# Kernel tuning notes

Hardware: AMD Instinct MI355X
Metric: run time of the kernel (lower is better)

## Reference

```python
import jax, jax.numpy as jnp
import numpy as np

NUM_HEADS = 16
LN_EPS = 1e-05


def setup_inputs() -> dict:
    key = jax.random.key(0)
    ks = jax.random.split(key, 10)
    B, S, H = 2, 2048, 1024
    s = 1.0 / np.sqrt(H)
    return {
        "hidden_states": jax.random.normal(ks[0], (B, S, H), dtype=jnp.float32),
        "Wq": jax.random.normal(ks[1], (H, H), dtype=jnp.float32) * s,
        "bq": jax.random.normal(ks[2], (H,), dtype=jnp.float32) * 0.02,
        "Wk": jax.random.normal(ks[3], (H, H), dtype=jnp.float32) * s,
        "bk": jax.random.normal(ks[4], (H,), dtype=jnp.float32) * 0.02,
        "Wv": jax.random.normal(ks[5], (H, H), dtype=jnp.float32) * s,
        "bv": jax.random.normal(ks[6], (H,), dtype=jnp.float32) * 0.02,
        "Wd": jax.random.normal(ks[7], (H, H), dtype=jnp.float32) * s,
        "bd": jax.random.normal(ks[8], (H,), dtype=jnp.float32) * 0.02,
        "ln_gamma": jnp.ones((H,), dtype=jnp.float32),
        "ln_beta": jnp.zeros((H,), dtype=jnp.float32),
    }


def reference(hidden_states, Wq, bq, Wk, bk, Wv, bv, Wd, bd, ln_gamma, ln_beta):
    B, S, H = hidden_states.shape
    nh = NUM_HEADS
    hd = H // nh

    # QKV projections (torch Linear: x @ W.T + b), split heads -> [B, nh, S, hd]
    def proj(W, b):
        y = jnp.einsum('bsh,oh->bso', hidden_states, W) + b
        return y.reshape(B, S, nh, hd).transpose(0, 2, 1, 3)

    q = proj(Wq, bq)
    k = proj(Wk, bk)
    v = proj(Wv, bv)

    # scaled dot-product attention: [B, nh, S, S]
    scores = jnp.einsum('bhqd,bhkd->bhqk', q, k) / jnp.sqrt(jnp.float32(hd))
    probs = jax.nn.softmax(scores, axis=-1)
    ctx = jnp.einsum('bhqk,bhkd->bhqd', probs, v)  # [B, nh, S, hd]
    ctx = ctx.transpose(0, 2, 1, 3).reshape(B, S, H)

    # output dense + residual + LayerNorm
    attn_out = jnp.einsum('bsh,oh->bso', ctx, Wd) + bd
    x = attn_out + hidden_states
    mu = jnp.mean(x, axis=-1, keepdims=True)
    var = jnp.mean(jnp.square(x - mu), axis=-1, keepdims=True)
    return (x - mu) * jax.lax.rsqrt(var + LN_EPS) * ln_gamma + ln_beta
```

## Files before the change

### kernel.cpp

```cpp
#include <hip/hip_runtime.h>

constexpr int kH    = 1024;
constexpr int kSEQ  = 2048;
constexpr int kBATCH= 2;
constexpr int kNH   = 16;
constexpr int kHD   = 64;
constexpr int kM    = 4096;

typedef _Float16 h8  __attribute__((ext_vector_type(8)));
typedef _Float16 h4  __attribute__((ext_vector_type(4)));
typedef float   f32x4 __attribute__((ext_vector_type(4)));

static __device__ __forceinline__ f32x4 mfma16(h8 a, h8 b, f32x4 c) {
  return __builtin_amdgcn_mfma_f32_16x16x32_f16(a, b, c, 0, 0, 0);
}

static __device__ __forceinline__ void gll16(const _Float16* g, _Float16* l) {
  __builtin_amdgcn_global_load_lds(
      (const __attribute__((address_space(1))) void*)g,
      (__attribute__((address_space(3))) void*)l, 16, 0, 0);
}

#define QSCALE 0.18033688011112042f
#define C0INIT (-5.770780163555854f)

__global__ __launch_bounds__(256) void cvt_all(
    const float* __restrict__ X,  const float* __restrict__ Wq,
    const float* __restrict__ Wk, const float* __restrict__ Wv,
    const float* __restrict__ Wd,
    _Float16* __restrict__ Xh,  _Float16* __restrict__ Wqh,
    _Float16* __restrict__ Wkh, _Float16* __restrict__ Wvh,
    _Float16* __restrict__ Wdh)
{
  int i = blockIdx.x * 256 + threadIdx.x;
  const float* src; _Float16* dst; int off;
  if (i < (kM * kH) / 4) {
    src = X; dst = Xh; off = i;
  } else {
    int j = i - (kM * kH) / 4;
    int w = j >> 18;
    off = j & 262143;
    src = (w == 0) ? Wq : (w == 1) ? Wk : (w == 2) ? Wv : Wd;
    dst = (w == 0) ? Wqh : (w == 1) ? Wkh : (w == 2) ? Wvh : Wdh;
  }
  float4 v = reinterpret_cast<const float4*>(src)[off];
  h4 o;
  o[0] = (_Float16)v.x; o[1] = (_Float16)v.y;
  o[2] = (_Float16)v.z; o[3] = (_Float16)v.w;
  reinterpret_cast<h4*>(dst)[off] = o;
}

__global__ __launch_bounds__(256, 2) void qkv_gemm(
    const _Float16* __restrict__ Xh,
    const _Float16* __restrict__ Wq, const _Float16* __restrict__ Wk,
    const _Float16* __restrict__ Wv,
    const float* __restrict__ bq, const float* __restrict__ bk,
    const float* __restrict__ bv,
    _Float16* __restrict__ Qo, _Float16* __restrict__ Ko, _Float16* __restrict__ Vo)
{
  const int proj = blockIdx.z;
  const _Float16* W   = (proj == 0) ? Wq : ((proj == 1) ? Wk : Wv);
  const float*    bias= (proj == 0) ? bq : ((proj == 1) ? bk : bv);
  _Float16*       Out = (proj == 0) ? Qo : ((proj == 1) ? Ko : Vo);

  const int m0 = blockIdx.y * 128, n0 = blockIdx.x * 128;
  __shared__ __align__(16) char qsmem[32768];
  _Float16* const As = (_Float16*)qsmem;
  _Float16* const Bs = (_Float16*)(qsmem + 16384);
  _Float16* const Lt = (_Float16*)qsmem;

  const int tid  = threadIdx.x;
  const int wave = tid >> 6, lane = tid & 63, quad = lane >> 4, l16 = lane & 15;
  const int mw = (wave & 1) * 64, nw = (wave >> 1) * 64;

  f32x4 acc[4][4] = {};
  const int grow = wave * 32 + (lane >> 2);
  const int gcol = (lane & 3) * 8;
  const _Float16* Ag = Xh + (size_t)(m0 + grow) * kH + gcol;
  const _Float16* Bg = W  + (size_t)(n0 + grow) * kH + gcol;

  {
    gll16(Ag,            &As[wave * 1024]);
    gll16(Ag + 16 * kH,  &As[wave * 1024 + 512]);
    gll16(Bg,            &Bs[wave * 1024]);
    gll16(Bg + 16 * kH,  &Bs[wave * 1024 + 512]);
  }

  for (int k = 0; k < 32; ++k) {
    const int cur = k & 1;
    __syncthreads();
    if (k < 31) {
      const int k0 = (k + 1) * 32, nb = cur ^ 1;
      gll16(Ag + k0,           &As[nb * 4096 + wave * 1024]);
      gll16(Ag + 16 * kH + k0, &As[nb * 4096 + wave * 1024 + 512]);
      gll16(Bg + k0,           &Bs[nb * 4096 + wave * 1024]);
      gll16(Bg + 16 * kH + k0, &Bs[nb * 4096 + wave * 1024 + 512]);
    }
    h8 af[4], bf[4];
    #pragma unroll
    for (int mi = 0; mi < 4; ++mi)
      af[mi] = *reinterpret_cast<const h8*>(&As[cur * 4096 + (mw + mi * 16 + l16) * 32 + quad * 8]);
    #pragma unroll
    for (int ni = 0; ni < 4; ++ni)
      bf[ni] = *reinterpret_cast<const h8*>(&Bs[cur * 4096 + (nw + ni * 16 + l16) * 32 + quad * 8]);
    #pragma unroll
    for (int mi = 0; mi < 4; ++mi)
      #pragma unroll
      for (int ni = 0; ni < 4; ++ni)
        acc[mi][ni] = mfma16(af[mi], bf[ni], acc[mi][ni]);
  }

  if (proj != 2) {
    #pragma unroll
    for (int mi = 0; mi < 4; ++mi)
    #pragma unroll
    for (int ni = 0; ni < 4; ++ni) {
      const int ng = n0 + nw + ni * 16 + l16;
      const float bv_ = bias[ng];
      const int hh = ng >> 6, dd = ng & 63;
      #pragma unroll
      for (int r = 0; r < 4; ++r) {
        const int mg = m0 + mw + mi * 16 + quad * 4 + r;
        float val = acc[mi][ni][r] + bv_;
        if (proj == 0) val *= QSCALE;
        const int bb = mg >> 11, srow = mg & 2047;
        Out[(((size_t)(bb * kNH + hh) * kSEQ) + srow) * kHD + dd] = (_Float16)val;
      }
    }
  } else {
    __syncthreads();
    #pragma unroll
    for (int mi = 0; mi < 4; ++mi)
    #pragma unroll
    for (int ni = 0; ni < 4; ++ni) {
      const int ng = n0 + nw + ni * 16 + l16;
      const float bv_ = bias[ng];
      const int nl = nw + ni * 16 + l16;
      const int c16 = (mw >> 3) + mi * 2 + (quad >> 1);
      const int cs = c16 ^ (nl & 15);
      h4 pp;
      pp[0] = (_Float16)(acc[mi][ni][0] + bv_);
      pp[1] = (_Float16)(acc[mi][ni][1] + bv_);
      pp[2] = (_Float16)(acc[mi][ni][2] + bv_);
      pp[3] = (_Float16)(acc[mi][ni][3] + bv_);
      *reinterpret_cast<h4*>(&Lt[nl * 128 + cs * 8 + (quad & 1) * 4]) = pp;
    }
    __syncthreads();
    const int bb = m0 >> 11, srow0 = m0 & 2047;
    const int nl2 = tid >> 1, half = tid & 1;
    const int ng2 = n0 + nl2, hh2 = ng2 >> 6, dd2 = ng2 & 63;
    _Float16* dst = Out + ((size_t)(bb * kNH + hh2) * kHD + dd2) * kSEQ
                        + srow0 + half * 64;
    #pragma unroll
    for (int j = 0; j < 8; ++j) {
      const int c = half * 8 + j;
      const int cs = c ^ (nl2 & 15);
      *reinterpret_cast<h8*>(dst + j * 8) =
          *reinterpret_cast<const h8*>(&Lt[nl2 * 128 + cs * 8]);
    }
  }
}

__global__ __launch_bounds__(512, 4) void attn_kernel(
    const _Float16* __restrict__ Q, const _Float16* __restrict__ K,
    const _Float16* __restrict__ Vt, _Float16* __restrict__ Ctx)
{
  const int qt = blockIdx.x, bh = blockIdx.y;
  const int tid = threadIdx.x;
  const int wave = tid >> 6, lane = tid & 63, quad = lane >> 4, l16 = lane & 15;
  const int sw = l16 & 7;
  const int qw = wave & 3;
  const int wg = wave >> 2;

  __shared__ __align__(16) char smem[61440];
  _Float16* const Kl = (_Float16*)smem;
  _Float16* const Vl = (_Float16*)(smem + 16384);
  _Float16* const Pl = (_Float16*)(smem + 32768);
  float* const Ored = (float*)smem;
  float* const Lred = (float*)(smem + 34816);

  const _Float16* Qb = Q  + (size_t)bh * kSEQ * kHD;
  const _Float16* Kb = K  + (size_t)bh * kSEQ * kHD;
  const _Float16* Vb = Vt + (size_t)bh * kHD * kSEQ;

  const int qbase = qt * 128 + qw * 32;
  h8 qf[2][2];
  #pragma unroll
  for (int qh = 0; qh < 2; ++qh)
    #pragma unroll
    for (int dh = 0; dh < 2; ++dh)
      qf[qh][dh] = *reinterpret_cast<const h8*>(
          &Qb[(size_t)(qbase + qh * 16 + l16) * kHD + dh * 32 + quad * 8]);

  const int srow0  = lane >> 3;
  const int schunk = (lane & 7) ^ srow0;
  const int krow   = wave * 8 + srow0;
  const _Float16* Kg = Kb + (size_t)krow * kHD + schunk * 8;
  const _Float16* Vg = Vb + (size_t)krow * kSEQ + schunk * 8;
  _Float16* const PlW = Pl + wave * 1792;

  float l_acc[2] = {0.f, 0.f};
  f32x4 o[2][4] = {};

  gll16(Kg, &Kl[(wave * 8) * 64]);
  gll16(Vg, &Vl[(wave * 8) * 64]);

  for (int kt = 0; kt < kSEQ / 64; ++kt) {
    const int cur = kt & 1;
    __syncthreads();
    if (kt + 1 < kSEQ / 64) {
      const int nb = cur ^ 1;
      const size_t ko = (size_t)(kt + 1) * 64;
      gll16(Kg + ko * kHD, &Kl[nb * 4096 + (wave * 8) * 64]);
      gll16(Vg + ko,       &Vl[nb * 4096 + (wave * 8) * 64]);
    }
    const _Float16* Kc = Kl + cur * 4096;
    const _Float16* Vc = Vl + cur * 4096;

    h8 ka[2][2];
    #pragma unroll
    for (int nt = 0; nt < 2; ++nt) {
      const int keyl = wg * 32 + nt * 16 + l16;
      ka[nt][0] = *reinterpret_cast<const h8*>(&Kc[keyl * 64 + ((quad    ) ^ sw) * 8]);
      ka[nt][1] = *reinterpret_cast<const h8*>(&Kc[keyl * 64 + ((quad ^ 4) ^ sw) * 8]);
    }
    f32x4 s[2][2];
    __builtin_amdgcn_s_setprio(1);
    #pragma unroll
    for (int nt = 0; nt < 2; ++nt)
      #pragma unroll
      for (int qh = 0; qh < 2; ++qh) {
        f32x4 a = {C0INIT, C0INIT, C0INIT, C0INIT};
        a = mfma16(ka[nt][0], qf[qh][0], a);
        a = mfma16(ka[nt][1], qf[qh][1], a);
        s[nt][qh] = a;
      }
    __builtin_amdgcn_s_setprio(0);

    #pragma unroll
    for (int nt = 0; nt < 2; ++nt)
      #pragma unroll
      for (int qh = 0; qh < 2; ++qh) {
        float e0 = __builtin_amdgcn_exp2f(s[nt][qh][0]);
        float e1 = __builtin_amdgcn_exp2f(s[nt][qh][1]);
        float e2 = __builtin_amdgcn_exp2f(s[nt][qh][2]);
        float e3 = __builtin_amdgcn_exp2f(s[nt][qh][3]);
        l_acc[qh] += (e0 + e1) + (e2 + e3);
        h4 pp;
        pp[0] = (_Float16)e0; pp[1] = (_Float16)e1;
        pp[2] = (_Float16)e2; pp[3] = (_Float16)e3;
        const int c = nt * 2 + (quad >> 1);
        *reinterpret_cast<h4*>(&PlW[(qh * 16 + l16) * 56 + c * 8 + (quad & 1) * 4]) = pp;
      }

    h8 pa0 = *reinterpret_cast<const h8*>(&PlW[(     l16) * 56 + quad * 8]);
    h8 pa1 = *reinterpret_cast<const h8*>(&PlW[(16 + l16) * 56 + quad * 8]);
    const int cs = ((wg * 4 + quad) ^ sw) * 8;
    h8 vb0 = *reinterpret_cast<const h8*>(&Vc[(0 * 16 + l16) * 64 + cs]);
    h8 vb1 = *reinterpret_cast<const h8*>(&Vc[(1 * 16 + l16) * 64 + cs]);
    h8 vb2 = *reinterpret_cast<const h8*>(&Vc[(2 * 16 + l16) * 64 + cs]);
    h8 vb3 = *reinterpret_cast<const h8*>(&Vc[(3 * 16 + l16) * 64 + cs]);
    __builtin_amdgcn_s_setprio(1);
    o[0][0] = mfma16(pa0, vb0, o[0][0]);
    o[1][0] = mfma16(pa1, vb0, o[1][0]);
    o[0][1] = mfma16(pa0, vb1, o[0][1]);
    o[1][1] = mfma16(pa1, vb1, o[1][1]);
    o[0][2] = mfma16(pa0, vb2, o[0][2]);
    o[1][2] = mfma16(pa1, vb2, o[1][2]);
    o[0][3] = mfma16(pa0, vb3, o[0][3]);
    o[1][3] = mfma16(pa1, vb3, o[1][3]);
    __builtin_amdgcn_s_setprio(0);
  }

  float li[2] = {l_acc[0], l_acc[1]};
  #pragma unroll
  for (int qh = 0; qh < 2; ++qh) {
    li[qh] += __shfl_xor(li[qh], 16);
    li[qh] += __shfl_xor(li[qh], 32);
  }

  __syncthreads();
  if (wg == 1) {
    float* myO = Ored + (qw * 64 + lane) * 34;
    #pragma unroll
    for (int qh = 0; qh < 2; ++qh)
      #pragma unroll
      for (int dt = 0; dt < 4; ++dt) {
        reinterpret_cast<float2*>(&myO[qh * 16 + dt * 4])[0] =
            reinterpret_cast<const float2*>(&o[qh][dt])[0];
        reinterpret_cast<float2*>(&myO[qh * 16 + dt * 4 + 2])[0] =
            reinterpret_cast<const float2*>(&o[qh][dt])[1];
      }
    if (quad == 0) {
      Lred[(qw * 2 + 0) * 16 + l16] = li[0];
      Lred[(qw * 2 + 1) * 16 + l16] = li[1];
    }
  }
  __syncthreads();
  if (wg == 1) return;

  const float* pO = Ored + (qw * 64 + lane) * 34;
  #pragma unroll
  for (int qh = 0; qh < 2; ++qh) {
    #pragma unroll
    for (int dt = 0; dt < 4; ++dt) {
      float2 a = reinterpret_cast<const float2*>(&pO[qh * 16 + dt * 4])[0];
      float2 b2 = reinterpret_cast<const float2*>(&pO[qh * 16 + dt * 4 + 2])[0];
      o[qh][dt][0] += a.x;  o[qh][dt][1] += a.y;
      o[qh][dt][2] += b2.x; o[qh][dt][3] += b2.y;
    }
    li[qh] = 1.f / (li[qh] + Lred[(qw * 2 + qh) * 16 + l16]);
  }
  const int b = bh >> 4, hh = bh & 15;
  #pragma unroll
  for (int qh = 0; qh < 2; ++qh)
    #pragma unroll
    for (int r = 0; r < 4; ++r) {
      const float linv = __shfl(li[qh], quad * 4 + r);
      const int srow = qbase + qh * 16 + quad * 4 + r;
      #pragma unroll
      for (int dt = 0; dt < 4; ++dt) {
        const int col = hh * kHD + dt * 16 + l16;
        Ctx[((size_t)(b * kSEQ + srow)) * kH + col] = (_Float16)(o[qh][dt][r] * linv);
      }
    }
}

__global__ __launch_bounds__(256, 2) void dense_gemm(
    const _Float16* __restrict__ A, const _Float16* __restrict__ W,
    const float* __restrict__ bias, const float* __restrict__ resid,
    float* __restrict__ Out)
{
  const int m0 = blockIdx.y * 128, n0 = blockIdx.x * 64;
  __shared__ __align__(16) _Float16 As[2][128 * 32];
  __shared__ __align__(16) _Float16 Bs[2][64 * 32];
  const int tid  = threadIdx.x;
  const int wave = tid >> 6, lane = tid & 63, quad = lane >> 4, l16 = lane & 15;
  const int mw = (wave & 1) * 64, nw = (wave >> 1) * 32;
  f32x4 acc[4][2] = {};
  const int growA = wave * 32 + (lane >> 2);
  const int growB = wave * 16 + (lane >> 2);
  const int gcol = (lane & 3) * 8;
  const _Float16* Ag = A + (size_t)(m0 + growA) * kH + gcol;
  const _Float16* Bg = W + (size_t)(n0 + growB) * kH + gcol;

  {
    gll16(Ag,           &As[0][wave * 1024]);
    gll16(Ag + 16 * kH, &As[0][wave * 1024 + 512]);
    gll16(Bg,           &Bs[0][wave * 512]);
  }

  for (int k = 0; k < 32; ++k) {
    const int cur = k & 1;
    __syncthreads();
    if (k < 31) {
      const int k0 = (k + 1) * 32, nb = cur ^ 1;
      gll16(Ag + k0,           &As[nb][wave * 1024]);
      gll16(Ag + 16 * kH + k0, &As[nb][wave * 1024 + 512]);
      gll16(Bg + k0,           &Bs[nb][wave * 512]);
    }
    h8 af[4], bf[2];
    #pragma unroll
    for (int mi = 0; mi < 4; ++mi)
      af[mi] = *reinterpret_cast<const h8*>(&As[cur][(mw + mi * 16 + l16) * 32 + quad * 8]);
    #pragma unroll
    for (int ni = 0; ni < 2; ++ni)
      bf[ni] = *reinterpret_cast<const h8*>(&Bs[cur][(nw + ni * 16 + l16) * 32 + quad * 8]);
    #pragma unroll
    for (int mi = 0; mi < 4; ++mi)
      #pragma unroll
      for (int ni = 0; ni < 2; ++ni)
        acc[mi][ni] = mfma16(af[mi], bf[ni], acc[mi][ni]);
  }
  #pragma unroll
  for (int mi = 0; mi < 4; ++mi)
  #pragma unroll
  for (int ni = 0; ni < 2; ++ni) {
    const int ng = n0 + nw + ni * 16 + l16;
    const float bv_ = bias[ng];
    #pragma unroll
    for (int r = 0; r < 4; ++r) {
      const int mg = m0 + mw + mi * 16 + quad * 4 + r;
      Out[(size_t)mg * kH + ng] = acc[mi][ni][r] + bv_ + resid[(size_t)mg * kH + ng];
    }
  }
}

__global__ __launch_bounds__(256) void ln_kernel(const float* __restrict__ Tmp,
    const float* __restrict__ gamma, const float* __restrict__ beta,
    float* __restrict__ out)
{
  const int row = blockIdx.x;
  const float4 v = reinterpret_cast<const float4*>(Tmp + (size_t)row * kH)[threadIdx.x];
  float s  = v.x + v.y + v.z + v.w;
  float ss = v.x * v.x + v.y * v.y + v.z * v.z + v.w * v.w;
  #pragma unroll
  for (int off = 32; off > 0; off >>= 1) {
    s  += __shfl_down(s, off);
    ss += __shfl_down(ss, off);
  }
  __shared__ float red[8];
  const int wave = threadIdx.x >> 6, lane = threadIdx.x & 63;
  if (lane == 0) { red[wave] = s; red[4 + wave] = ss; }
  __syncthreads();
  s  = red[0] + red[1] + red[2] + red[3];
  ss = red[4] + red[5] + red[6] + red[7];
  const float mu   = s * (1.f / kH);
  const float var  = ss * (1.f / kH) - mu * mu;
  const float rstd = rsqrtf(var + 1e-5f);
  const float4 g  = reinterpret_cast<const float4*>(gamma)[threadIdx.x];
  const float4 bb = reinterpret_cast<const float4*>(beta)[threadIdx.x];
  float4 o;
  o.x = (v.x - mu) * rstd * g.x + bb.x;
  o.y = (v.y - mu) * rstd * g.y + bb.y;
  o.z = (v.z - mu) * rstd * g.z + bb.z;
  o.w = (v.w - mu) * rstd * g.w + bb.w;
  reinterpret_cast<float4*>(out + (size_t)row * kH)[threadIdx.x] = o;
}

extern "C" void kernel_launch(void* const* d_in, const int* in_sizes, int n_in,
                              void* d_out, int out_size, void* d_ws, size_t ws_size,
                              hipStream_t stream) {
  const float* hs    = (const float*)d_in[0];
  const float* Wq    = (const float*)d_in[1];
  const float* bq    = (const float*)d_in[2];
  const float* Wk    = (const float*)d_in[3];
  const float* bk    = (const float*)d_in[4];
  const float* Wv    = (const float*)d_in[5];
  const float* bv    = (const float*)d_in[6];
  const float* Wd    = (const float*)d_in[7];
  const float* bd    = (const float*)d_in[8];
  const float* gamma = (const float*)d_in[9];
  const float* beta  = (const float*)d_in[10];
  float* out = (float*)d_out;

  char* ws = (char*)d_ws;
  _Float16* Xh  = (_Float16*)(ws + 0);
  _Float16* Wqh = (_Float16*)(ws + 8388608);
  _Float16* Wkh = (_Float16*)(ws + 10485760);
  _Float16* Wvh = (_Float16*)(ws + 12582912);
  _Float16* Wdh = (_Float16*)(ws + 14680064);
  _Float16* Qh  = (_Float16*)(ws + 16777216);
  _Float16* Kh  = (_Float16*)(ws + 25165824);
  _Float16* Vth = (_Float16*)(ws + 33554432);
  _Float16* Ch  = (_Float16*)(ws + 41943040);
  float*    Tmp = (float*)Qh;

  cvt_all<<<8192, 256, 0, stream>>>(hs, Wq, Wk, Wv, Wd, Xh, Wqh, Wkh, Wvh, Wdh);
  qkv_gemm<<<dim3(kH / 128, kM / 128, 3), 256, 0, stream>>>(
      Xh, Wqh, Wkh, Wvh, bq, bk, bv, Qh, Kh, Vth);
  attn_kernel<<<dim3(kSEQ / 128, kBATCH * kNH), 512, 0, stream>>>(Qh, Kh, Vth, Ch);
  dense_gemm<<<dim3(kH / 64, kM / 128), 256, 0, stream>>>(Ch, Wdh, bd, hs, Tmp);
  ln_kernel<<<kM, 256, 0, stream>>>(Tmp, gamma, beta, out);
}
```

Before: 204.3 us.

## Keep softmax probabilities in registers and permute V reads to match

Removes the per-wave LDS round trip for the probability tile. The exp results are packed directly into the MFMA A-operand registers, and the V operand is gathered with a matching permuted key order as two 4-element LDS reads. This drops the P buffer from shared memory, which shrinks LDS use and may raise occupancy. In exchange, the V reads become narrower b64 loads instead of b128 ones.

```diff
diff --git a/kernel.cpp b/kernel.cpp
--- a/kernel.cpp
+++ b/kernel.cpp
@@ -172,10 +172,9 @@
   const int qw = wave & 3;
   const int wg = wave >> 2;
 
-  __shared__ __align__(16) char smem[61440];
+  __shared__ __align__(16) char smem[35328];
   _Float16* const Kl = (_Float16*)smem;
   _Float16* const Vl = (_Float16*)(smem + 16384);
-  _Float16* const Pl = (_Float16*)(smem + 32768);
   float* const Ored = (float*)smem;
   float* const Lred = (float*)(smem + 34816);
 
@@ -197,7 +196,12 @@
   const int krow   = wave * 8 + srow0;
   const _Float16* Kg = Kb + (size_t)krow * kHD + schunk * 8;
   const _Float16* Vg = Vb + (size_t)krow * kSEQ + schunk * 8;
-  _Float16* const PlW = Pl + wave * 1792;
+
+  const int sA = 4 * wg + (quad >> 1);
+  const int sB = sA + 2;
+  const int hA = (quad & 1) * 4;
+  const int offA = ((sA ^ sw) << 3) + hA;
+  const int offB = ((sB ^ sw) << 3) + hA;
 
   float l_acc[2] = {0.f, 0.f};
   f32x4 o[2][4] = {};
@@ -237,38 +241,38 @@
       }
     __builtin_amdgcn_s_setprio(0);
 
-    #pragma unroll
-    for (int nt = 0; nt < 2; ++nt)
-      #pragma unroll
-      for (int qh = 0; qh < 2; ++qh) {
-        float e0 = __builtin_amdgcn_exp2f(s[nt][qh][0]);
-        float e1 = __builtin_amdgcn_exp2f(s[nt][qh][1]);
-        float e2 = __builtin_amdgcn_exp2f(s[nt][qh][2]);
-        float e3 = __builtin_amdgcn_exp2f(s[nt][qh][3]);
-        l_acc[qh] += (e0 + e1) + (e2 + e3);
-        h4 pp;
-        pp[0] = (_Float16)e0; pp[1] = (_Float16)e1;
-        pp[2] = (_Float16)e2; pp[3] = (_Float16)e3;
-        const int c = nt * 2 + (quad >> 1);
-        *reinterpret_cast<h4*>(&PlW[(qh * 16 + l16) * 56 + c * 8 + (quad & 1) * 4]) = pp;
-      }
-
-    h8 pa0 = *reinterpret_cast<const h8*>(&PlW[(     l16) * 56 + quad * 8]);
-    h8 pa1 = *reinterpret_cast<const h8*>(&PlW[(16 + l16) * 56 + quad * 8]);
-    const int cs = ((wg * 4 + quad) ^ sw) * 8;
-    h8 vb0 = *reinterpret_cast<const h8*>(&Vc[(0 * 16 + l16) * 64 + cs]);
-    h8 vb1 = *reinterpret_cast<const h8*>(&Vc[(1 * 16 + l16) * 64 + cs]);
-    h8 vb2 = *reinterpret_cast<const h8*>(&Vc[(2 * 16 + l16) * 64 + cs]);
-    h8 vb3 = *reinterpret_cast<const h8*>(&Vc[(3 * 16 + l16) * 64 + cs]);
+    h8 pa[2];
+    #pragma unroll
+    for (int qh = 0; qh < 2; ++qh) {
+      float e00 = __builtin_amdgcn_exp2f(s[0][qh][0]);
+      float e01 = __builtin_amdgcn_exp2f(s[0][qh][1]);
+      float e02 = __builtin_amdgcn_exp2f(s[0][qh][2]);
+      float e03 = __builtin_amdgcn_exp2f(s[0][qh][3]);
+      float e10 = __builtin_amdgcn_exp2f(s[1][qh][0]);
+      float e11 = __builtin_amdgcn_exp2f(s[1][qh][1]);
+      float e12 = __builtin_amdgcn_exp2f(s[1][qh][2]);
+      float e13 = __builtin_amdgcn_exp2f(s[1][qh][3]);
+      l_acc[qh] += ((e00 + e01) + (e02 + e03)) + ((e10 + e11) + (e12 + e13));
+      h8 p;
+      p[0] = (_Float16)e00; p[1] = (_Float16)e01;
+      p[2] = (_Float16)e02; p[3] = (_Float16)e03;
+      p[4] = (_Float16)e10; p[5] = (_Float16)e11;
+      p[6] = (_Float16)e12; p[7] = (_Float16)e13;
+      pa[qh] = p;
+    }
+
     __builtin_amdgcn_s_setprio(1);
-    o[0][0] = mfma16(pa0, vb0, o[0][0]);
-    o[1][0] = mfma16(pa1, vb0, o[1][0]);
-    o[0][1] = mfma16(pa0, vb1, o[0][1]);
-    o[1][1] = mfma16(pa1, vb1, o[1][1]);
-    o[0][2] = mfma16(pa0, vb2, o[0][2]);
-    o[1][2] = mfma16(pa1, vb2, o[1][2]);
-    o[0][3] = mfma16(pa0, vb3, o[0][3]);
-    o[1][3] = mfma16(pa1, vb3, o[1][3]);
+    #pragma unroll
+    for (int dt = 0; dt < 4; ++dt) {
+      const _Float16* vr = &Vc[(dt * 16 + l16) * 64];
+      h4 va = *reinterpret_cast<const h4*>(vr + offA);
+      h4 vbb = *reinterpret_cast<const h4*>(vr + offB);
+      h8 v8;
+      v8[0] = va[0];  v8[1] = va[1];  v8[2] = va[2];  v8[3] = va[3];
+      v8[4] = vbb[0]; v8[5] = vbb[1]; v8[6] = vbb[2]; v8[7] = vbb[3];
+      o[0][dt] = mfma16(pa[0], v8, o[0][dt]);
+      o[1][dt] = mfma16(pa[1], v8, o[1][dt]);
+    }
     __builtin_amdgcn_s_setprio(0);
   }
 
```

New measurement: 203.6 us. Within noise of the previous version (-0.4%).
